# Optimization experiments

Measured on AMD Instinct MI355X. Metric: run time of the kernel, lower is better.

## Reference

```python
import jax, jax.numpy as jnp
import numpy as np

N, H, M, B = 64, 64, 32, 16384
relu = jax.nn.relu


def setup_inputs() -> dict:
    key = jax.random.key(0)
    ks = jax.random.split(key, 10)
    s = 0.05
    x = jax.random.normal(ks[0], (B, N), dtype=jnp.float32)
    # stacked per-node weights (torch Linear applies x @ W.T, W: [out, in])
    W1a = jax.random.normal(ks[1], (N, H, N), dtype=jnp.float32) * s   # directed net layer 1
    W1b = jax.random.normal(ks[2], (N, M, H), dtype=jnp.float32) * s   # directed net layer 2
    W2a = jax.random.normal(ks[3], (N, H, N), dtype=jnp.float32) * s   # bi-directed net layer 1
    W2b = jax.random.normal(ks[4], (N, M, H), dtype=jnp.float32) * s   # bi-directed net layer 2
    W3a = jax.random.normal(ks[5], (N, H, 2 * M + N), dtype=jnp.float32) * s  # fuse layer 1
    b3a = jax.random.normal(ks[6], (N, H), dtype=jnp.float32) * s
    W3b = jax.random.normal(ks[7], (N, 1, H), dtype=jnp.float32) * s          # fuse layer 2
    b3b = jax.random.normal(ks[8], (N, 1), dtype=jnp.float32) * s
    return {"x": x, "W1a": W1a, "W1b": W1b, "W2a": W2a, "W2b": W2b,
            "W3a": W3a, "b3a": b3a, "W3b": W3b, "b3b": b3b}


def reference(x, W1a, W1b, W2a, W2b, W3a, b3a, W3b, b3b):
    Bsz, n = x.shape
    eye = jnp.eye(n, dtype=x.dtype)
    off = 1.0 - eye  # filter_1; adjacency at init is also (ones - eye), so mask is idempotent
    # inputs_1_dag / inputs_1_bi: [B, N, N] per-node masked copies of x
    x1 = jnp.einsum('bn,in->bin', x, off)
    # inputs_2: [B, N, N] with x[b,i] on the diagonal of row i
    x2 = eye[None, :, :] * x[:, None, :]
    # directed branch: ReLU(Linear) -> ReLU(Linear), batched over node i
    r1 = relu(jnp.einsum('bih,imh->bim', relu(jnp.einsum('bin,ihn->bih', x1, W1a)), W1b))
    # bi-directed branch (same masked input at init)
    r2 = relu(jnp.einsum('bih,imh->bim', relu(jnp.einsum('bin,ihn->bih', x1, W2a)), W2b))
    feat = jnp.concatenate([r1, r2, x2], axis=2)  # [B, N, 2M+N]
    h = relu(jnp.einsum('bik,ihk->bih', feat, W3a) + b3a[None])
    out = relu(jnp.einsum('bih,ioh->bio', h, W3b) + b3b[None])  # [B, N, 1]
    return out[..., 0]  # [B, N] causal derivative
```

## Files before the change

kernel.cpp:

```cpp
#include <hip/hip_runtime.h>


typedef short bf16x8 __attribute__((ext_vector_type(8)));
typedef float f32x4  __attribute__((ext_vector_type(4)));
typedef unsigned int u32x4 __attribute__((ext_vector_type(4)));
typedef unsigned int u32x2 __attribute__((ext_vector_type(2)));

#define PITCH_S    72
#define WAVE_LDS_S 3456

__device__ __forceinline__ unsigned int pack2(float a, float b) {
    union { float f; unsigned int u; } ua, ub; ua.f = a; ub.f = b;
    return __builtin_amdgcn_perm(ub.u + 0x8000u, ua.u + 0x8000u, 0x07060302u);
}

__device__ __forceinline__ f32x4 mfma16(bf16x8 a, bf16x8 b, f32x4 c) {
    return __builtin_amdgcn_mfma_f32_16x16x32_bf16(a, b, c, 0, 0, 0);
}

__device__ __forceinline__ bf16x8 cvt_frag(const float* __restrict__ p) {
    f32x4 f0 = *(const f32x4*)p;
    f32x4 f1 = *(const f32x4*)(p + 4);
    union { u32x4 u; bf16x8 v; } r;
    r.u[0] = pack2(f0[0], f0[1]);
    r.u[1] = pack2(f0[2], f0[3]);
    r.u[2] = pack2(f1[0], f1[1]);
    r.u[3] = pack2(f1[2], f1[3]);
    return r.v;
}

__device__ __forceinline__ bf16x8 cvt_frag_m(const float* __restrict__ p, const unsigned int* M) {
    f32x4 f0 = *(const f32x4*)p;
    f32x4 f1 = *(const f32x4*)(p + 4);
    union { u32x4 u; bf16x8 v; } r;
    r.u[0] = pack2(f0[0], f0[1]) & M[0];
    r.u[1] = pack2(f0[2], f0[3]) & M[1];
    r.u[2] = pack2(f1[0], f1[1]) & M[2];
    r.u[3] = pack2(f1[2], f1[3]) & M[3];
    return r.v;
}

__global__ __launch_bounds__(256) void prep_x(const float* __restrict__ x,
                                              unsigned short* __restrict__ xb) {
    int j = (blockIdx.x * 256 + threadIdx.x) * 8;
    f32x4 a = *(const f32x4*)&x[j];
    f32x4 b = *(const f32x4*)&x[j + 4];
    u32x4 r = { pack2(a[0], a[1]), pack2(a[2], a[3]), pack2(b[0], b[1]), pack2(b[2], b[3]) };
    *(u32x4*)&xb[j] = r;
}

__global__ __launch_bounds__(256, 2) void main_kernel(
    const float* __restrict__ x,
    const float* __restrict__ W1a, const float* __restrict__ W1b,
    const float* __restrict__ W2a, const float* __restrict__ W2b,
    const float* __restrict__ W3a, const float* __restrict__ b3a,
    const float* __restrict__ W3b, const float* __restrict__ b3b,
    const unsigned short* __restrict__ xb,
    float* __restrict__ out)
{
    __shared__ unsigned short lds[4 * WAVE_LDS_S];

    const int i    = blockIdx.x & 63;
    const int bg   = blockIdx.x >> 6;
    const int tid  = threadIdx.x;
    const int w    = tid >> 6;
    const int lane = tid & 63;
    const int q    = lane >> 4;
    const int c0   = lane & 15;

    unsigned int M[2][4];
    {
        const unsigned int halfmask = (i & 1) ? 0x0000FFFFu : 0xFFFF0000u;
        const int dz = (i >> 1) & 3;
        #pragma unroll
        for (int s = 0; s < 2; ++s) {
            bool hit = ((i >> 3) == s * 4 + q);
            #pragma unroll
            for (int d = 0; d < 4; ++d)
                M[s][d] = (hit && d == dz) ? halfmask : 0xFFFFFFFFu;
        }
    }

    bf16x8 A1[4][2], A2[4][2];
    {
        const float* p1 = W1a + (i << 12);
        const float* p2 = W2a + (i << 12);
        #pragma unroll
        for (int t = 0; t < 4; ++t)
            #pragma unroll
            for (int s = 0; s < 2; ++s) {
                int off = (((t << 4) + c0) << 6) + (s << 5) + (q << 3);
                A1[t][s] = cvt_frag_m(p1 + off, M[s]);
                A2[t][s] = cvt_frag_m(p2 + off, M[s]);
            }
    }
    bf16x8 F1[2][2], F2[2][2];
    {
        const float* p1 = W1b + (i << 11);
        const float* p2 = W2b + (i << 11);
        #pragma unroll
        for (int t = 0; t < 2; ++t)
            #pragma unroll
            for (int s = 0; s < 2; ++s) {
                int off = (((t << 4) + c0) << 6) + (s << 5) + (q << 3);
                F1[t][s] = cvt_frag(p1 + off);
                F2[t][s] = cvt_frag(p2 + off);
            }
    }
    bf16x8 A3[4][2];
    {
        const float* p3 = W3a + (i << 13);
        #pragma unroll
        for (int t = 0; t < 4; ++t)
            #pragma unroll
            for (int s = 0; s < 2; ++s)
                A3[t][s] = cvt_frag(p3 + (((t << 4) + c0) << 7) + (s << 5) + (q << 3));
    }
    f32x4 b3av[4], w3xv[4], w3bv[4];
    #pragma unroll
    for (int t = 0; t < 4; ++t) {
        int h0 = (i << 6) + (t << 4) + (q << 2);
        b3av[t] = *(const f32x4*)&b3a[h0];
        w3bv[t] = *(const f32x4*)&W3b[h0];
        #pragma unroll
        for (int r = 0; r < 4; ++r)
            w3xv[t][r] = W3a[(i << 13) + (((t << 4) + (q << 2) + r) << 7) + 64 + i];
    }
    const float bb = b3b[i];

    unsigned short* Hw       = &lds[w * WAVE_LDS_S + c0 * PITCH_S + (q << 2)];
    const unsigned short* Hr = &lds[w * WAVE_LDS_S + c0 * PITCH_S + (q << 3)];

    const int rbase0 = (((bg << 2) + w) << 9);

    int row = rbase0 + c0;
    bf16x8 XB0 = *(const bf16x8*)&xb[(row << 6) + (q << 3)];
    bf16x8 XB1 = *(const bf16x8*)&xb[(row << 6) + 32 + (q << 3)];
    float   xd = x[(row << 6) + i];

    for (int k = 0; k < 32; ++k) {
        int nrow = rbase0 + ((k < 31 ? k + 1 : 31) << 4) + c0;
        bf16x8 nXB0 = *(const bf16x8*)&xb[(nrow << 6) + (q << 3)];
        bf16x8 nXB1 = *(const bf16x8*)&xb[(nrow << 6) + 32 + (q << 3)];
        float   nxd = x[(nrow << 6) + i];

        #pragma unroll
        for (int t = 0; t < 4; ++t) {
            f32x4 a1 = {0.f, 0.f, 0.f, 0.f}, a2 = {0.f, 0.f, 0.f, 0.f};
            a1 = mfma16(A1[t][0], XB0, a1); a1 = mfma16(A1[t][1], XB1, a1);
            a2 = mfma16(A2[t][0], XB0, a2); a2 = mfma16(A2[t][1], XB1, a2);
            u32x2 w1 = { pack2(fmaxf(a1[0], 0.f), fmaxf(a1[1], 0.f)),
                         pack2(fmaxf(a1[2], 0.f), fmaxf(a1[3], 0.f)) };
            u32x2 w2 = { pack2(fmaxf(a2[0], 0.f), fmaxf(a2[1], 0.f)),
                         pack2(fmaxf(a2[2], 0.f), fmaxf(a2[3], 0.f)) };
            *(u32x2*)&Hw[t << 4]          = w1;
            *(u32x2*)&Hw[1152 + (t << 4)] = w2;
        }
        bf16x8 HB0 = *(const bf16x8*)&Hr[0];
        bf16x8 HB1 = *(const bf16x8*)&Hr[32];
        bf16x8 GB0 = *(const bf16x8*)&Hr[1152];
        bf16x8 GB1 = *(const bf16x8*)&Hr[1152 + 32];

        #pragma unroll
        for (int t = 0; t < 2; ++t) {
            f32x4 a1 = {0.f, 0.f, 0.f, 0.f}, a2 = {0.f, 0.f, 0.f, 0.f};
            a1 = mfma16(F1[t][0], HB0, a1); a1 = mfma16(F1[t][1], HB1, a1);
            a2 = mfma16(F2[t][0], GB0, a2); a2 = mfma16(F2[t][1], GB1, a2);
            u32x2 w1 = { pack2(fmaxf(a1[0], 0.f), fmaxf(a1[1], 0.f)),
                         pack2(fmaxf(a1[2], 0.f), fmaxf(a1[3], 0.f)) };
            u32x2 w2 = { pack2(fmaxf(a2[0], 0.f), fmaxf(a2[1], 0.f)),
                         pack2(fmaxf(a2[2], 0.f), fmaxf(a2[3], 0.f)) };
            *(u32x2*)&Hw[2304 + (t << 4)]      = w1;
            *(u32x2*)&Hw[2304 + 32 + (t << 4)] = w2;
        }
        bf16x8 RB0 = *(const bf16x8*)&Hr[2304];
        bf16x8 RB1 = *(const bf16x8*)&Hr[2304 + 32];

        float p = 0.f;
        #pragma unroll
        for (int t = 0; t < 4; ++t) {
            f32x4 acc;
            #pragma unroll
            for (int r = 0; r < 4; ++r) acc[r] = fmaf(xd, w3xv[t][r], b3av[t][r]);
            acc = mfma16(A3[t][0], RB0, acc);
            acc = mfma16(A3[t][1], RB1, acc);
            #pragma unroll
            for (int r = 0; r < 4; ++r) p = fmaf(fmaxf(acc[r], 0.f), w3bv[t][r], p);
        }
        p += __shfl_xor(p, 16);
        p += __shfl_xor(p, 32);
        if (lane < 16) out[(row << 6) + i] = fmaxf(p + bb, 0.f);

        row = nrow; XB0 = nXB0; XB1 = nXB1; xd = nxd;
    }
}

extern "C" void kernel_launch(void* const* d_in, const int* in_sizes, int n_in,
                              void* d_out, int out_size, void* d_ws, size_t ws_size,
                              hipStream_t stream) {
    (void)in_sizes; (void)n_in; (void)out_size; (void)ws_size;
    const float* x   = (const float*)d_in[0];
    const float* W1a = (const float*)d_in[1];
    const float* W1b = (const float*)d_in[2];
    const float* W2a = (const float*)d_in[3];
    const float* W2b = (const float*)d_in[4];
    const float* W3a = (const float*)d_in[5];
    const float* b3a = (const float*)d_in[6];
    const float* W3b = (const float*)d_in[7];
    const float* b3b = (const float*)d_in[8];
    float* out = (float*)d_out;
    unsigned short* xb = (unsigned short*)d_ws;

    prep_x<<<512, 256, 0, stream>>>(x, xb);
    main_kernel<<<512, 256, 0, stream>>>(x, W1a, W1b, W2a, W2b, W3a, b3a, W3b, b3b, xb, out);
}
```

Measured before the change: 135.9 us.

## Keep inter-layer activations in registers by permuting weight K-fragments

Removes the per-wave LDS round trip between the MFMA layers. The K-dimension element order of the second- and third-layer weight fragments is permuted at load time so that MFMA output accumulators can be repacked directly into the next layer's B operand in registers. This drops the LDS writes and reads and their latency from every iteration. In exchange it holds more accumulator registers live, which could raise register pressure at two blocks per CU.

```diff
diff --git a/kernel.cpp b/kernel.cpp
--- a/kernel.cpp
+++ b/kernel.cpp
@@ -4,10 +4,6 @@
 typedef short bf16x8 __attribute__((ext_vector_type(8)));
 typedef float f32x4  __attribute__((ext_vector_type(4)));
 typedef unsigned int u32x4 __attribute__((ext_vector_type(4)));
-typedef unsigned int u32x2 __attribute__((ext_vector_type(2)));
-
-#define PITCH_S    72
-#define WAVE_LDS_S 3456
 
 __device__ __forceinline__ unsigned int pack2(float a, float b) {
     union { float f; unsigned int u; } ua, ub; ua.f = a; ub.f = b;
@@ -18,9 +14,19 @@
     return __builtin_amdgcn_mfma_f32_16x16x32_bf16(a, b, c, 0, 0, 0);
 }
 
-__device__ __forceinline__ bf16x8 cvt_frag(const float* __restrict__ p) {
-    f32x4 f0 = *(const f32x4*)p;
-    f32x4 f1 = *(const f32x4*)(p + 4);
+__device__ __forceinline__ bf16x8 pack_frag(f32x4 lo, f32x4 hi) {
+    union { u32x4 u; bf16x8 v; } r;
+    r.u[0] = pack2(fmaxf(lo[0], 0.f), fmaxf(lo[1], 0.f));
+    r.u[1] = pack2(fmaxf(lo[2], 0.f), fmaxf(lo[3], 0.f));
+    r.u[2] = pack2(fmaxf(hi[0], 0.f), fmaxf(hi[1], 0.f));
+    r.u[3] = pack2(fmaxf(hi[2], 0.f), fmaxf(hi[3], 0.f));
+    return r.v;
+}
+
+__device__ __forceinline__ bf16x8 cvt_frag2(const float* __restrict__ plo,
+                                            const float* __restrict__ phi) {
+    f32x4 f0 = *(const f32x4*)plo;
+    f32x4 f1 = *(const f32x4*)phi;
     union { u32x4 u; bf16x8 v; } r;
     r.u[0] = pack2(f0[0], f0[1]);
     r.u[1] = pack2(f0[2], f0[3]);
@@ -29,9 +35,11 @@
     return r.v;
 }
 
-__device__ __forceinline__ bf16x8 cvt_frag_m(const float* __restrict__ p, const unsigned int* M) {
-    f32x4 f0 = *(const f32x4*)p;
-    f32x4 f1 = *(const f32x4*)(p + 4);
+__device__ __forceinline__ bf16x8 cvt_frag2_m(const float* __restrict__ plo,
+                                              const float* __restrict__ phi,
+                                              const unsigned int* M) {
+    f32x4 f0 = *(const f32x4*)plo;
+    f32x4 f1 = *(const f32x4*)phi;
     union { u32x4 u; bf16x8 v; } r;
     r.u[0] = pack2(f0[0], f0[1]) & M[0];
     r.u[1] = pack2(f0[2], f0[3]) & M[1];
@@ -58,8 +66,6 @@
     const unsigned short* __restrict__ xb,
     float* __restrict__ out)
 {
-    __shared__ unsigned short lds[4 * WAVE_LDS_S];
-
     const int i    = blockIdx.x & 63;
     const int bg   = blockIdx.x >> 6;
     const int tid  = threadIdx.x;
@@ -90,8 +96,8 @@
             #pragma unroll
             for (int s = 0; s < 2; ++s) {
                 int off = (((t << 4) + c0) << 6) + (s << 5) + (q << 3);
-                A1[t][s] = cvt_frag_m(p1 + off, M[s]);
-                A2[t][s] = cvt_frag_m(p2 + off, M[s]);
+                A1[t][s] = cvt_frag2_m(p1 + off, p1 + off + 4, M[s]);
+                A2[t][s] = cvt_frag2_m(p2 + off, p2 + off + 4, M[s]);
             }
     }
     bf16x8 F1[2][2], F2[2][2];
@@ -102,9 +108,9 @@
         for (int t = 0; t < 2; ++t)
             #pragma unroll
             for (int s = 0; s < 2; ++s) {
-                int off = (((t << 4) + c0) << 6) + (s << 5) + (q << 3);
-                F1[t][s] = cvt_frag(p1 + off);
-                F2[t][s] = cvt_frag(p2 + off);
+                int base = (((t << 4) + c0) << 6) + (s << 5) + (q << 2);
+                F1[t][s] = cvt_frag2(p1 + base, p1 + base + 16);
+                F2[t][s] = cvt_frag2(p2 + base, p2 + base + 16);
             }
     }
     bf16x8 A3[4][2];
@@ -113,8 +119,10 @@
         #pragma unroll
         for (int t = 0; t < 4; ++t)
             #pragma unroll
-            for (int s = 0; s < 2; ++s)
-                A3[t][s] = cvt_frag(p3 + (((t << 4) + c0) << 7) + (s << 5) + (q << 3));
+            for (int s = 0; s < 2; ++s) {
+                int base = (((t << 4) + c0) << 7) + (s << 5) + (q << 2);
+                A3[t][s] = cvt_frag2(p3 + base, p3 + base + 16);
+            }
     }
     f32x4 b3av[4], w3xv[4], w3bv[4];
     #pragma unroll
@@ -128,9 +136,6 @@
     }
     const float bb = b3b[i];
 
-    unsigned short* Hw       = &lds[w * WAVE_LDS_S + c0 * PITCH_S + (q << 2)];
-    const unsigned short* Hr = &lds[w * WAVE_LDS_S + c0 * PITCH_S + (q << 3)];
-
     const int rbase0 = (((bg << 2) + w) << 9);
 
     int row = rbase0 + c0;
@@ -144,37 +149,31 @@
         bf16x8 nXB1 = *(const bf16x8*)&xb[(nrow << 6) + 32 + (q << 3)];
         float   nxd = x[(nrow << 6) + i];
 
+        f32x4 a1[4], a2[4];
         #pragma unroll
         for (int t = 0; t < 4; ++t) {
-            f32x4 a1 = {0.f, 0.f, 0.f, 0.f}, a2 = {0.f, 0.f, 0.f, 0.f};
-            a1 = mfma16(A1[t][0], XB0, a1); a1 = mfma16(A1[t][1], XB1, a1);
-            a2 = mfma16(A2[t][0], XB0, a2); a2 = mfma16(A2[t][1], XB1, a2);
-            u32x2 w1 = { pack2(fmaxf(a1[0], 0.f), fmaxf(a1[1], 0.f)),
-                         pack2(fmaxf(a1[2], 0.f), fmaxf(a1[3], 0.f)) };
-            u32x2 w2 = { pack2(fmaxf(a2[0], 0.f), fmaxf(a2[1], 0.f)),
-                         pack2(fmaxf(a2[2], 0.f), fmaxf(a2[3], 0.f)) };
-            *(u32x2*)&Hw[t << 4]          = w1;
-            *(u32x2*)&Hw[1152 + (t << 4)] = w2;
-        }
-        bf16x8 HB0 = *(const bf16x8*)&Hr[0];
-        bf16x8 HB1 = *(const bf16x8*)&Hr[32];
-        bf16x8 GB0 = *(const bf16x8*)&Hr[1152];
-        bf16x8 GB1 = *(const bf16x8*)&Hr[1152 + 32];
-
+            f32x4 z = {0.f, 0.f, 0.f, 0.f};
+            f32x4 u = mfma16(A1[t][0], XB0, z);
+            a1[t]   = mfma16(A1[t][1], XB1, u);
+            f32x4 v = mfma16(A2[t][0], XB0, z);
+            a2[t]   = mfma16(A2[t][1], XB1, v);
+        }
+        bf16x8 HB0 = pack_frag(a1[0], a1[1]);
+        bf16x8 HB1 = pack_frag(a1[2], a1[3]);
+        bf16x8 GB0 = pack_frag(a2[0], a2[1]);
+        bf16x8 GB1 = pack_frag(a2[2], a2[3]);
+
+        f32x4 b1[2], b2[2];
         #pragma unroll
         for (int t = 0; t < 2; ++t) {
-            f32x4 a1 = {0.f, 0.f, 0.f, 0.f}, a2 = {0.f, 0.f, 0.f, 0.f};
-            a1 = mfma16(F1[t][0], HB0, a1); a1 = mfma16(F1[t][1], HB1, a1);
-            a2 = mfma16(F2[t][0], GB0, a2); a2 = mfma16(F2[t][1], GB1, a2);
-            u32x2 w1 = { pack2(fmaxf(a1[0], 0.f), fmaxf(a1[1], 0.f)),
-                         pack2(fmaxf(a1[2], 0.f), fmaxf(a1[3], 0.f)) };
-            u32x2 w2 = { pack2(fmaxf(a2[0], 0.f), fmaxf(a2[1], 0.f)),
-                         pack2(fmaxf(a2[2], 0.f), fmaxf(a2[3], 0.f)) };
-            *(u32x2*)&Hw[2304 + (t << 4)]      = w1;
-            *(u32x2*)&Hw[2304 + 32 + (t << 4)] = w2;
-        }
-        bf16x8 RB0 = *(const bf16x8*)&Hr[2304];
-        bf16x8 RB1 = *(const bf16x8*)&Hr[2304 + 32];
+            f32x4 z = {0.f, 0.f, 0.f, 0.f};
+            f32x4 u = mfma16(F1[t][0], HB0, z);
+            b1[t]   = mfma16(F1[t][1], HB1, u);
+            f32x4 v = mfma16(F2[t][0], GB0, z);
+            b2[t]   = mfma16(F2[t][1], GB1, v);
+        }
+        bf16x8 RB0 = pack_frag(b1[0], b1[1]);
+        bf16x8 RB1 = pack_frag(b2[0], b2[1]);
 
         float p = 0.f;
         #pragma unroll
```

Measured after the change: 131.7 us. -3.1%, faster.
